# Kernel tuning notes

Measured on AMD Instinct MI355X. Metric: run time of the kernel, lower is better.

## Reference

```python
import jax, jax.numpy as jnp
import numpy as np

B, S, H = 4, 2048, 768
NUM_HEADS = 12
HEAD_DIM = H // NUM_HEADS


def setup_inputs() -> dict:
    key = jax.random.key(0)
    k1, k2, k3 = jax.random.split(key, 3)
    hidden_states = jax.random.normal(k1, (B, S, H), dtype=jnp.float32)
    # torch Linear weight [out,in]; store transposed [in,out] for x @ W
    w_qkv = jax.random.normal(k2, (H, 3 * H), dtype=jnp.float32) * (1.0 / np.sqrt(H))
    w_out = jax.random.normal(k3, (H, H), dtype=jnp.float32) * (1.0 / np.sqrt(H))
    return {"hidden_states": hidden_states, "w_qkv": w_qkv, "w_out": w_out}


def reference(hidden_states, w_qkv, w_out):
    b, s, h = hidden_states.shape
    qkv = hidden_states @ w_qkv                      # [b,s,3h]
    qkv = qkv.reshape(b, s, 3, NUM_HEADS, HEAD_DIM)
    qkv = jnp.transpose(qkv, (2, 0, 3, 1, 4))        # [3,b,nh,s,hd]
    q, k, v = qkv[0], qkv[1], qkv[2]
    scale = 1.0 / np.sqrt(HEAD_DIM).astype(np.float32)
    scores = jnp.einsum('bhqd,bhkd->bhqk', q, k) * scale   # [b,nh,s,s]
    causal = jnp.triu(jnp.ones((s, s), dtype=bool), k=1)
    scores = jnp.where(causal, jnp.float32(-jnp.inf), scores)
    attn = jax.nn.softmax(scores, axis=-1)
    # dropout is identity in eval mode
    out = jnp.einsum('bhqk,bhkd->bhqd', attn, v)      # [b,nh,s,hd]
    out = jnp.transpose(out, (0, 2, 1, 3)).reshape(b, s, h)
    return out @ w_out
```

## Files before the change

### kernel.cpp

```cpp
#include <hip/hip_runtime.h>
#include <stdint.h>

#define B_ 4
#define S_ 2048
#define H_ 768
#define NH_ 12
#define HD_ 64
#define BH_ (B_ * NH_)

#define QSCALE 0.18033688011112042f

typedef __attribute__((ext_vector_type(4))) float f32x4;
typedef __attribute__((ext_vector_type(8))) __bf16 bf16x8;
typedef __attribute__((ext_vector_type(8))) unsigned short ushort8;

__device__ __forceinline__ unsigned short bf16rne(float f) {
  union { float f; unsigned int u; } v;
  v.f = f;
  unsigned int u = v.u;
  return (unsigned short)((u + 0x7fffu + ((u >> 16) & 1u)) >> 16);
}

#if __has_builtin(__builtin_amdgcn_cvt_pk_bf16_f32)
__device__ __forceinline__ unsigned int pk2(float a, float b) {
  auto r = __builtin_amdgcn_cvt_pk_bf16_f32(a, b);
  return *(unsigned int*)&r;
}
#else
__device__ __forceinline__ unsigned int pk2(float a, float b) {
  return (unsigned int)bf16rne(a) | ((unsigned int)bf16rne(b) << 16);
}
#endif

#if __has_builtin(__builtin_amdgcn_exp2f)
#define EXP2F(x) __builtin_amdgcn_exp2f(x)
#else
#define EXP2F(x) exp2f(x)
#endif

__device__ __forceinline__ void gll16(const void* g, void* l) {
  __builtin_amdgcn_global_load_lds(
      (const __attribute__((address_space(1))) unsigned int*)g,
      (__attribute__((address_space(3))) unsigned int*)l, 16, 0, 0);
}

__device__ __forceinline__ void tconv_body(const float* __restrict__ in,
                                           unsigned short* __restrict__ out,
                                           int R, int C, int bx, int by,
                                           unsigned short (*tile)[72], int tid) {
  int c0 = bx * 64, r0 = by * 64;
#pragma unroll
  for (int i = 0; i < 4; ++i) {
    int c = i * 256 + tid;
    int row = c >> 4, col4 = (c & 15) * 4;
    float4 v = *(const float4*)(in + (size_t)(r0 + row) * C + c0 + col4);
    *(uint2*)(&tile[row][col4]) = (uint2){pk2(v.x, v.y), pk2(v.z, v.w)};
  }
  __syncthreads();
#pragma unroll
  for (int i = 0; i < 2; ++i) {
    int c = i * 256 + tid;
    int oc = c >> 3, r8 = (c & 7) * 8;
    ushort8 v;
#pragma unroll
    for (int j = 0; j < 8; ++j) v[j] = tile[r8 + j][oc];
    *(ushort8*)(out + (size_t)(c0 + oc) * R + r0 + r8) = v;
  }
}

__global__ __launch_bounds__(256) void prep_kernel(const float* __restrict__ hs,
                                                   const float* __restrict__ wqkv,
                                                   const float* __restrict__ wout,
                                                   unsigned short* __restrict__ Xbf,
                                                   unsigned short* __restrict__ Wqkvt,
                                                   unsigned short* __restrict__ Woutt) {
  __shared__ unsigned short tile[64][72];
  int bid = blockIdx.x, tid = threadIdx.x;
  if (bid < 3072) {
    int i = (bid * 256 + tid) * 8;
    const float4* p = (const float4*)(hs + i);
    float4 a = p[0], b = p[1];
    uint4 r = {pk2(a.x, a.y), pk2(a.z, a.w), pk2(b.x, b.y), pk2(b.z, b.w)};
    *(uint4*)(Xbf + i) = r;
  } else if (bid < 3504) {
    int idx = bid - 3072;
    tconv_body(wqkv, Wqkvt, 768, 2304, idx % 36, idx / 36, tile, tid);
  } else {
    int idx = bid - 3504;
    tconv_body(wout, Woutt, 768, 768, idx % 12, idx / 12, tile, tid);
  }
}

template <int MODE>
__device__ __forceinline__ void gemm_core(const unsigned short* __restrict__ A,
                                          const unsigned short* __restrict__ Bm,
                                          void* __restrict__ Cout, int N, int K,
                                          int bm, int bn,
                                          unsigned short* As, unsigned short* Bs) {
  int tid = threadIdx.x;
  int lane = tid & 63, wave = tid >> 6;
  int quad = lane >> 4, l16 = lane & 15;
  int wm = (wave & 1) * 64, wn = (wave >> 1) * 64;
  const unsigned short* Ag = A + (size_t)bm * 128 * K;
  const unsigned short* Bg = Bm + (size_t)bn * 128 * K;

  f32x4 zero = {0.f, 0.f, 0.f, 0.f};
  f32x4 acc[4][4];
#pragma unroll
  for (int mt = 0; mt < 4; ++mt)
#pragma unroll
    for (int nt = 0; nt < 4; ++nt) acc[mt][nt] = zero;

  for (int k0 = 0; k0 < K; k0 += 32) {
#pragma unroll
    for (int i = 0; i < 2; ++i) {
      int c = i * 256 + tid;
      int row = c >> 2, off = (c & 3) * 8;
      gll16(Ag + (size_t)row * K + k0 + off, As + c * 8);
      gll16(Bg + (size_t)row * K + k0 + off, Bs + c * 8);
    }
    __syncthreads();
    bf16x8 af[4], bf[4];
#pragma unroll
    for (int mt = 0; mt < 4; ++mt)
      af[mt] = *(const bf16x8*)(As + (wm + mt * 16 + l16) * 32 + quad * 8);
#pragma unroll
    for (int nt = 0; nt < 4; ++nt)
      bf[nt] = *(const bf16x8*)(Bs + (wn + nt * 16 + l16) * 32 + quad * 8);
#pragma unroll
    for (int mt = 0; mt < 4; ++mt)
#pragma unroll
      for (int nt = 0; nt < 4; ++nt) {
        if (MODE == 2)
          acc[mt][nt] = __builtin_amdgcn_mfma_f32_16x16x32_bf16(af[mt], bf[nt], acc[mt][nt], 0, 0, 0);
        else
          acc[mt][nt] = __builtin_amdgcn_mfma_f32_16x16x32_bf16(bf[nt], af[mt], acc[mt][nt], 0, 0, 0);
      }
    __syncthreads();
  }

  if (MODE == 0) {
    unsigned short* qkv = (unsigned short*)Cout;
    int which = (bn >= 6);
#pragma unroll
    for (int mt = 0; mt < 4; ++mt)
#pragma unroll
      for (int nt = 0; nt < 4; ++nt) {
        int f0 = bn * 128 + wn + nt * 16 + quad * 4;
        int tm = bm * 128 + wm + mt * 16 + l16;
        int rem = f0 - which * 768;
        int head = rem >> 6, d0 = rem & 63;
        int b = tm >> 11, s = tm & 2047;
        if (which == 0) {
          uint2 pkv = {pk2(acc[mt][nt][0] * QSCALE, acc[mt][nt][1] * QSCALE),
                       pk2(acc[mt][nt][2] * QSCALE, acc[mt][nt][3] * QSCALE)};
          *(uint2*)(qkv + (((size_t)b * NH_ + head) * S_ + s) * HD_ + d0) = pkv;
        } else {
          uint2 pkv = {pk2(acc[mt][nt][0], acc[mt][nt][1]),
                       pk2(acc[mt][nt][2], acc[mt][nt][3])};
          int dd0 = (((d0 >> 3) ^ (s & 7)) << 3) | (d0 & 7);
          *(uint2*)(qkv + (((size_t)(BH_ + b * NH_ + head)) * S_ + s) * HD_ + dd0) = pkv;
        }
      }
  } else if (MODE == 2) {
    unsigned short* vt = (unsigned short*)Cout;
#pragma unroll
    for (int mt = 0; mt < 4; ++mt)
#pragma unroll
      for (int nt = 0; nt < 4; ++nt) {
        int f = bn * 128 + wn + nt * 16 + l16;
        int t0 = bm * 128 + wm + mt * 16 + quad * 4;
        int rem = f - 1536;
        int head = rem >> 6, d = rem & 63;
        int b = t0 >> 11, s0 = t0 & 2047;
        int tile = s0 >> 6, sin = s0 & 63;
        int pos = (((sin >> 3) ^ (d & 7)) << 3) | (sin & 7);
        uint2 pkv = {pk2(acc[mt][nt][0], acc[mt][nt][1]),
                     pk2(acc[mt][nt][2], acc[mt][nt][3])};
        *(uint2*)(vt + (((size_t)(b * NH_ + head)) * HD_ + d) * S_ + tile * 64 + pos) = pkv;
      }
  } else {
    float* outp = (float*)Cout;
#pragma unroll
    for (int mt = 0; mt < 4; ++mt)
#pragma unroll
      for (int nt = 0; nt < 4; ++nt) {
        int f0 = bn * 128 + wn + nt * 16 + quad * 4;
        int tm = bm * 128 + wm + mt * 16 + l16;
        *(f32x4*)(outp + (size_t)tm * N + f0) = acc[mt][nt];
      }
  }
}

__global__ __launch_bounds__(256) void gemm_qkv(const unsigned short* __restrict__ A,
                                                const unsigned short* __restrict__ Bm,
                                                unsigned short* __restrict__ QK,
                                                unsigned short* __restrict__ Vt) {
  __shared__ unsigned short As[128 * 32];
  __shared__ unsigned short Bs[128 * 32];
  int bm = blockIdx.x, bn = blockIdx.y;
  if (bn < 12)
    gemm_core<0>(A, Bm, QK, 2304, 768, bm, bn, As, Bs);
  else
    gemm_core<2>(A, Bm, Vt, 2304, 768, bm, bn, As, Bs);
}

__global__ __launch_bounds__(256) void gemm_out(const unsigned short* __restrict__ A,
                                                const unsigned short* __restrict__ Bm,
                                                float* __restrict__ Cout) {
  __shared__ unsigned short As[128 * 32];
  __shared__ unsigned short Bs[128 * 32];
  gemm_core<1>(A, Bm, Cout, 768, 768, blockIdx.x, blockIdx.y, As, Bs);
}

__global__ __launch_bounds__(512, 6) void attn_kernel(const unsigned short* __restrict__ Q,
                                                      const unsigned short* __restrict__ Kg,
                                                      const unsigned short* __restrict__ Vt,
                                                      unsigned short* __restrict__ O) {
  __shared__ unsigned short Ks[2][64 * 64];
  __shared__ unsigned short Vs[2][64 * 64];
  __shared__ unsigned short Ps[8][16 * 64];
  const int pi_[16] = {0, 1, 3, 5, 7, 9, 11, 13, 15, 14, 12, 10, 8, 6, 4, 2};
  int bh = blockIdx.x;
  int y = blockIdx.y;
  int qt = pi_[(bh + y) & 15];
  int tid = threadIdx.x, lane = tid & 63, wave = tid >> 6;
  int quad = lane >> 4, l16 = lane & 15;
  const unsigned short* Qp = Q + (size_t)bh * S_ * HD_;
  int q0 = qt * 128;
  int qrow = q0 + wave * 16 + l16;
  int kmax_w = (q0 + wave * 16 + 15) >> 6;
  int kmax_b = 2 * qt + 1;

  const unsigned short* kSrc = Kg + (size_t)bh * S_ * HD_ + (tid >> 3) * HD_ + (tid & 7) * 8;
  const unsigned short* vSrc = Vt + (size_t)bh * HD_ * S_ + (size_t)(tid >> 3) * S_ + (tid & 7) * 8;
  unsigned short* kDst = &Ks[0][tid * 8];
  unsigned short* vDst = &Vs[0][tid * 8];

  auto stage = [&](int t, int buf) {
    gll16(kSrc + (size_t)t * 4096, kDst + buf * 4096);
    gll16(vSrc + t * 64, vDst + buf * 4096);
  };

  stage(0, 0);

  bf16x8 qf[2];
#pragma unroll
  for (int ks = 0; ks < 2; ++ks)
    qf[ks] = *(const bf16x8*)(Qp + (size_t)qrow * HD_ + ks * 32 + quad * 8);

  bf16x8 ones;
#pragma unroll
  for (int j = 0; j < 8; ++j) ones[j] = (__bf16)1.0f;

  int fo[8];
#pragma unroll
  for (int ks = 0; ks < 2; ++ks)
#pragma unroll
    for (int nt = 0; nt < 4; ++nt)
      fo[ks * 4 + nt] = (nt * 16 + l16) * 64 + (((ks * 4 + quad) ^ (l16 & 7)) << 3);
  int po[2];
#pragma unroll
  for (int ks = 0; ks < 2; ++ks)
    po[ks] = l16 * 64 + (((ks * 4 + quad) ^ (l16 & 7)) << 3);
  int pw[4];
#pragma unroll
  for (int nt = 0; nt < 4; ++nt)
    pw[nt] = l16 * 64 + ((((nt * 2 + (quad >> 1)) ^ (l16 & 7)) << 3) | ((quad & 1) * 4));
  unsigned short* psW = &Ps[wave][0];

  f32x4 zero = {0.f, 0.f, 0.f, 0.f};
  float l_i = 0.f;
  f32x4 o[4];
#pragma unroll
  for (int nt = 0; nt < 4; ++nt) o[nt] = zero;

  auto body = [&](int t, const unsigned short* Kb, const unsigned short* Vb) {
    f32x4 sf[4];
#pragma unroll
    for (int nt = 0; nt < 4; ++nt) sf[nt] = zero;
#pragma unroll
    for (int ks = 0; ks < 2; ++ks)
#pragma unroll
      for (int nt = 0; nt < 4; ++nt) {
        bf16x8 kf = *(const bf16x8*)(Kb + fo[ks * 4 + nt]);
        sf[nt] = __builtin_amdgcn_mfma_f32_16x16x32_bf16(kf, qf[ks], sf[nt], 0, 0, 0);
      }

    if (t == kmax_w) {
#pragma unroll
      for (int nt = 0; nt < 4; ++nt)
#pragma unroll
        for (int r = 0; r < 4; ++r)
          if (t * 64 + nt * 16 + quad * 4 + r > qrow) sf[nt][r] = -1e30f;
    }

#pragma unroll
    for (int nt = 0; nt < 4; ++nt) {
      uint2 pkv = {pk2(EXP2F(sf[nt][0]), EXP2F(sf[nt][1])),
                   pk2(EXP2F(sf[nt][2]), EXP2F(sf[nt][3]))};
      *(uint2*)(psW + pw[nt]) = pkv;
    }

    f32x4 rsv = zero;
#pragma unroll
    for (int ks = 0; ks < 2; ++ks) {
      bf16x8 pf = *(const bf16x8*)(psW + po[ks]);
      rsv = __builtin_amdgcn_mfma_f32_16x16x32_bf16(ones, pf, rsv, 0, 0, 0);
#pragma unroll
      for (int nt = 0; nt < 4; ++nt) {
        bf16x8 vf = *(const bf16x8*)(Vb + fo[ks * 4 + nt]);
        o[nt] = __builtin_amdgcn_mfma_f32_16x16x32_bf16(vf, pf, o[nt], 0, 0, 0);
      }
    }
    l_i += rsv[0];
  };

  for (int t = 0; t <= kmax_b; t += 2) {
    __syncthreads();
    stage(t + 1, 1);
    if (t <= kmax_w) body(t, &Ks[0][0], &Vs[0][0]);
    __syncthreads();
    if (t + 2 <= kmax_b) stage(t + 2, 0);
    if (t + 1 <= kmax_w) body(t + 1, &Ks[1][0], &Vs[1][0]);
  }

  float inv = 1.f / l_i;
  int b = bh / NH_, h = bh % NH_;
#pragma unroll
  for (int nt = 0; nt < 4; ++nt) {
    uint2 pkv = {pk2(o[nt][0] * inv, o[nt][1] * inv),
                 pk2(o[nt][2] * inv, o[nt][3] * inv)};
    int d0 = nt * 16 + quad * 4;
    *(uint2*)(O + ((size_t)b * S_ + qrow) * H_ + h * HD_ + d0) = pkv;
  }
}

extern "C" void kernel_launch(void* const* d_in, const int* in_sizes, int n_in,
                              void* d_out, int out_size, void* d_ws, size_t ws_size,
                              hipStream_t stream) {
  (void)in_sizes; (void)n_in; (void)out_size; (void)ws_size;
  const float* hs = (const float*)d_in[0];
  const float* wqkv = (const float*)d_in[1];
  const float* wout = (const float*)d_in[2];
  float* out = (float*)d_out;

  unsigned short* Xbf = (unsigned short*)d_ws;
  unsigned short* Wqkvt = Xbf + (size_t)8192 * 768;
  unsigned short* Woutt = Wqkvt + (size_t)2304 * 768;
  unsigned short* QK = Woutt + (size_t)768 * 768;
  unsigned short* Vt = QK + (size_t)2 * BH_ * S_ * HD_;
  unsigned short* Attn = Xbf;

  prep_kernel<<<3648, 256, 0, stream>>>(hs, wqkv, wout, Xbf, Wqkvt, Woutt);
  gemm_qkv<<<dim3(64, 18), 256, 0, stream>>>(Xbf, Wqkvt, QK, Vt);
  attn_kernel<<<dim3(48, 16), 512, 0, stream>>>(QK, QK + (size_t)BH_ * S_ * HD_, Vt, Attn);
  gemm_out<<<dim3(64, 6), 256, 0, stream>>>(Attn, Woutt, out);
}
```

Before: 197.9 us.

## Split attention key tiles across wave pairs and balance causal work with paired query tiles

The attention kernel now uses 64-row query tiles, and each block processes two of them (y and 31-y), so every block does about the same amount of causal work. Within a tile, pairs of waves split each 64-key block into halves, and the partial outputs and row sums are combined through shared memory at the end. This removes the lookup-table tile permutation and the per-wave uneven kmax handling. In exchange it adds a shared-memory reduction, extra barriers, and a barrier on every key tile. The launch grid must match 16 y-blocks per head, which is not shown.

```diff
diff --git a/kernel.cpp b/kernel.cpp
--- a/kernel.cpp
+++ b/kernel.cpp
@@ -217,38 +217,28 @@
                                                       const unsigned short* __restrict__ Kg,
                                                       const unsigned short* __restrict__ Vt,
                                                       unsigned short* __restrict__ O) {
-  __shared__ unsigned short Ks[2][64 * 64];
-  __shared__ unsigned short Vs[2][64 * 64];
-  __shared__ unsigned short Ps[8][16 * 64];
-  const int pi_[16] = {0, 1, 3, 5, 7, 9, 11, 13, 15, 14, 12, 10, 8, 6, 4, 2};
+  __shared__ __align__(16) unsigned short smem[24576];
+  unsigned short* Ks = smem;
+  unsigned short* Vs = smem + 8192;
+  unsigned short* Ps = smem + 16384;
+
   int bh = blockIdx.x;
   int y = blockIdx.y;
-  int qt = pi_[(bh + y) & 15];
   int tid = threadIdx.x, lane = tid & 63, wave = tid >> 6;
   int quad = lane >> 4, l16 = lane & 15;
+  int grp = wave >> 1, par = wave & 1;
   const unsigned short* Qp = Q + (size_t)bh * S_ * HD_;
-  int q0 = qt * 128;
-  int qrow = q0 + wave * 16 + l16;
-  int kmax_w = (q0 + wave * 16 + 15) >> 6;
-  int kmax_b = 2 * qt + 1;
 
   const unsigned short* kSrc = Kg + (size_t)bh * S_ * HD_ + (tid >> 3) * HD_ + (tid & 7) * 8;
   const unsigned short* vSrc = Vt + (size_t)bh * HD_ * S_ + (size_t)(tid >> 3) * S_ + (tid & 7) * 8;
-  unsigned short* kDst = &Ks[0][tid * 8];
-  unsigned short* vDst = &Vs[0][tid * 8];
+  unsigned short* kDst = &Ks[tid * 8];
+  unsigned short* vDst = &Vs[tid * 8];
 
   auto stage = [&](int t, int buf) {
     gll16(kSrc + (size_t)t * 4096, kDst + buf * 4096);
     gll16(vSrc + t * 64, vDst + buf * 4096);
   };
 
-  stage(0, 0);
-
-  bf16x8 qf[2];
-#pragma unroll
-  for (int ks = 0; ks < 2; ++ks)
-    qf[ks] = *(const bf16x8*)(Qp + (size_t)qrow * HD_ + ks * 32 + quad * 8);
-
   bf16x8 ones;
 #pragma unroll
   for (int j = 0; j < 8; ++j) ones[j] = (__bf16)1.0f;
@@ -259,80 +249,99 @@
 #pragma unroll
     for (int nt = 0; nt < 4; ++nt)
       fo[ks * 4 + nt] = (nt * 16 + l16) * 64 + (((ks * 4 + quad) ^ (l16 & 7)) << 3);
-  int po[2];
-#pragma unroll
-  for (int ks = 0; ks < 2; ++ks)
-    po[ks] = l16 * 64 + (((ks * 4 + quad) ^ (l16 & 7)) << 3);
-  int pw[4];
-#pragma unroll
-  for (int nt = 0; nt < 4; ++nt)
-    pw[nt] = l16 * 64 + ((((nt * 2 + (quad >> 1)) ^ (l16 & 7)) << 3) | ((quad & 1) * 4));
-  unsigned short* psW = &Ps[wave][0];
+  int po = l16 * 64 + (((par * 4 + quad) ^ (l16 & 7)) << 3);
+  int pw[2];
+#pragma unroll
+  for (int ntl = 0; ntl < 2; ++ntl) {
+    int ntp = par * 2 + ntl;
+    pw[ntl] = l16 * 64 + ((((ntp * 2 + (quad >> 1)) ^ (l16 & 7)) << 3) | ((quad & 1) * 4));
+  }
+  unsigned short* psW = &Ps[wave * 1024];
 
   f32x4 zero = {0.f, 0.f, 0.f, 0.f};
-  float l_i = 0.f;
-  f32x4 o[4];
-#pragma unroll
-  for (int nt = 0; nt < 4; ++nt) o[nt] = zero;
-
-  auto body = [&](int t, const unsigned short* Kb, const unsigned short* Vb) {
-    f32x4 sf[4];
-#pragma unroll
-    for (int nt = 0; nt < 4; ++nt) sf[nt] = zero;
+  int b = bh / NH_, h = bh % NH_;
+
+#pragma unroll 1
+  for (int pass = 0; pass < 2; ++pass) {
+    int qt = pass ? (31 - y) : y;
+    int q0 = qt * 64;
+    int qrow = q0 + grp * 16 + l16;
+
+    __syncthreads();
+    stage(0, 0);
+
+    bf16x8 qf[2];
 #pragma unroll
     for (int ks = 0; ks < 2; ++ks)
-#pragma unroll
-      for (int nt = 0; nt < 4; ++nt) {
-        bf16x8 kf = *(const bf16x8*)(Kb + fo[ks * 4 + nt]);
-        sf[nt] = __builtin_amdgcn_mfma_f32_16x16x32_bf16(kf, qf[ks], sf[nt], 0, 0, 0);
-      }
-
-    if (t == kmax_w) {
-#pragma unroll
-      for (int nt = 0; nt < 4; ++nt)
-#pragma unroll
-        for (int r = 0; r < 4; ++r)
-          if (t * 64 + nt * 16 + quad * 4 + r > qrow) sf[nt][r] = -1e30f;
+      qf[ks] = *(const bf16x8*)(Qp + (size_t)qrow * HD_ + ks * 32 + quad * 8);
+
+    f32x4 o[4];
+#pragma unroll
+    for (int nt = 0; nt < 4; ++nt) o[nt] = zero;
+    f32x4 rsum = zero;
+
+    for (int t = 0; t <= qt; ++t) {
+      __syncthreads();
+      if (t < qt) stage(t + 1, (t + 1) & 1);
+      const unsigned short* Kb = Ks + (t & 1) * 4096;
+      const unsigned short* Vb = Vs + (t & 1) * 4096;
+
+      f32x4 sf[2];
+      sf[0] = zero; sf[1] = zero;
+#pragma unroll
+      for (int ks = 0; ks < 2; ++ks)
+#pragma unroll
+        for (int ntl = 0; ntl < 2; ++ntl) {
+          bf16x8 kf = *(const bf16x8*)(Kb + fo[ks * 4 + (par * 2 + ntl)]);
+          sf[ntl] = __builtin_amdgcn_mfma_f32_16x16x32_bf16(kf, qf[ks], sf[ntl], 0, 0, 0);
+        }
+
+      if (t == qt) {
+#pragma unroll
+        for (int ntl = 0; ntl < 2; ++ntl)
+#pragma unroll
+          for (int r = 0; r < 4; ++r)
+            if ((par * 2 + ntl) * 16 + quad * 4 + r > grp * 16 + l16) sf[ntl][r] = -1e30f;
+      }
+
+#pragma unroll
+      for (int ntl = 0; ntl < 2; ++ntl) {
+        uint2 pkv = {pk2(EXP2F(sf[ntl][0]), EXP2F(sf[ntl][1])),
+                     pk2(EXP2F(sf[ntl][2]), EXP2F(sf[ntl][3]))};
+        *(uint2*)(psW + pw[ntl]) = pkv;
+      }
+
+      bf16x8 pf = *(const bf16x8*)(psW + po);
+      rsum = __builtin_amdgcn_mfma_f32_16x16x32_bf16(ones, pf, rsum, 0, 0, 0);
+#pragma unroll
+      for (int nt = 0; nt < 4; ++nt) {
+        bf16x8 vf = *(const bf16x8*)(Vb + fo[par * 4 + nt]);
+        o[nt] = __builtin_amdgcn_mfma_f32_16x16x32_bf16(vf, pf, o[nt], 0, 0, 0);
+      }
     }
-
-#pragma unroll
-    for (int nt = 0; nt < 4; ++nt) {
-      uint2 pkv = {pk2(EXP2F(sf[nt][0]), EXP2F(sf[nt][1])),
-                   pk2(EXP2F(sf[nt][2]), EXP2F(sf[nt][3]))};
-      *(uint2*)(psW + pw[nt]) = pkv;
+    float l = rsum[0];
+
+    __syncthreads();
+    float* sc = (float*)smem + (size_t)(grp * 64 + lane) * 20;
+    if (par) {
+#pragma unroll
+      for (int nt = 0; nt < 4; ++nt) *(f32x4*)(sc + nt * 4) = o[nt];
+      sc[16] = l;
     }
-
-    f32x4 rsv = zero;
-#pragma unroll
-    for (int ks = 0; ks < 2; ++ks) {
-      bf16x8 pf = *(const bf16x8*)(psW + po[ks]);
-      rsv = __builtin_amdgcn_mfma_f32_16x16x32_bf16(ones, pf, rsv, 0, 0, 0);
-#pragma unroll
-      for (int nt = 0; nt < 4; ++nt) {
-        bf16x8 vf = *(const bf16x8*)(Vb + fo[ks * 4 + nt]);
-        o[nt] = __builtin_amdgcn_mfma_f32_16x16x32_bf16(vf, pf, o[nt], 0, 0, 0);
+    __syncthreads();
+    if (!par) {
+#pragma unroll
+      for (int nt = 0; nt < 4; ++nt) o[nt] += *(const f32x4*)(sc + nt * 4);
+      l += sc[16];
+      float inv = 1.f / l;
+#pragma unroll
+      for (int nt = 0; nt < 4; ++nt) {
+        uint2 pkv = {pk2(o[nt][0] * inv, o[nt][1] * inv),
+                     pk2(o[nt][2] * inv, o[nt][3] * inv)};
+        int d0 = nt * 16 + quad * 4;
+        *(uint2*)(O + ((size_t)b * S_ + qrow) * H_ + h * HD_ + d0) = pkv;
       }
     }
-    l_i += rsv[0];
-  };
-
-  for (int t = 0; t <= kmax_b; t += 2) {
-    __syncthreads();
-    stage(t + 1, 1);
-    if (t <= kmax_w) body(t, &Ks[0][0], &Vs[0][0]);
-    __syncthreads();
-    if (t + 2 <= kmax_b) stage(t + 2, 0);
-    if (t + 1 <= kmax_w) body(t + 1, &Ks[1][0], &Vs[1][0]);
-  }
-
-  float inv = 1.f / l_i;
-  int b = bh / NH_, h = bh % NH_;
-#pragma unroll
-  for (int nt = 0; nt < 4; ++nt) {
-    uint2 pkv = {pk2(o[nt][0] * inv, o[nt][1] * inv),
-                 pk2(o[nt][2] * inv, o[nt][3] * inv)};
-    int d0 = nt * 16 + quad * 4;
-    *(uint2*)(O + ((size_t)b * S_ + qrow) * H_ + h * HD_ + d0) = pkv;
   }
 }
 
```

Result: slower. 224.7 us (+13.6%).

## Switch attention to 32x32x16 MFMA with four waves of 32 query rows

Applied to the files above, without the earlier changes.

Rewrites the attention kernel to use 32x32x16 bf16 MFMA tiles instead of 16x16x32. Each of four waves now handles 32 query rows, so a block is 256 threads rather than 512. Staging loads, the P scratch layout, causal masking indices and output writes are remapped to match. The larger tiles raise the MFMA work per LDS fragment load, at the cost of more accumulator registers per thread and fewer waves per block to hide latency.

```diff
diff --git a/kernel.cpp b/kernel.cpp
--- a/kernel.cpp
+++ b/kernel.cpp
@@ -11,6 +11,7 @@
 #define QSCALE 0.18033688011112042f
 
 typedef __attribute__((ext_vector_type(4))) float f32x4;
+typedef __attribute__((ext_vector_type(16))) float f32x16;
 typedef __attribute__((ext_vector_type(8))) __bf16 bf16x8;
 typedef __attribute__((ext_vector_type(8))) unsigned short ushort8;
 
@@ -213,107 +214,105 @@
   gemm_core<1>(A, Bm, Cout, 768, 768, blockIdx.x, blockIdx.y, As, Bs);
 }
 
-__global__ __launch_bounds__(512, 6) void attn_kernel(const unsigned short* __restrict__ Q,
+__global__ __launch_bounds__(256, 3) void attn_kernel(const unsigned short* __restrict__ Q,
                                                       const unsigned short* __restrict__ Kg,
                                                       const unsigned short* __restrict__ Vt,
                                                       unsigned short* __restrict__ O) {
   __shared__ unsigned short Ks[2][64 * 64];
   __shared__ unsigned short Vs[2][64 * 64];
-  __shared__ unsigned short Ps[8][16 * 64];
+  __shared__ unsigned short Ps[4][32 * 64];
   const int pi_[16] = {0, 1, 3, 5, 7, 9, 11, 13, 15, 14, 12, 10, 8, 6, 4, 2};
   int bh = blockIdx.x;
   int y = blockIdx.y;
   int qt = pi_[(bh + y) & 15];
   int tid = threadIdx.x, lane = tid & 63, wave = tid >> 6;
-  int quad = lane >> 4, l16 = lane & 15;
+  int l32 = lane & 31, h = lane >> 5;
   const unsigned short* Qp = Q + (size_t)bh * S_ * HD_;
   int q0 = qt * 128;
-  int qrow = q0 + wave * 16 + l16;
-  int kmax_w = (q0 + wave * 16 + 15) >> 6;
+  int qrow = q0 + wave * 32 + l32;
+  int kmax_w = (q0 + wave * 32 + 31) >> 6;
   int kmax_b = 2 * qt + 1;
 
-  const unsigned short* kSrc = Kg + (size_t)bh * S_ * HD_ + (tid >> 3) * HD_ + (tid & 7) * 8;
-  const unsigned short* vSrc = Vt + (size_t)bh * HD_ * S_ + (size_t)(tid >> 3) * S_ + (tid & 7) * 8;
-  unsigned short* kDst = &Ks[0][tid * 8];
-  unsigned short* vDst = &Vs[0][tid * 8];
+  const unsigned short* kS = Kg + (size_t)bh * S_ * HD_ + (tid >> 3) * HD_ + (tid & 7) * 8;
+  const unsigned short* vS = Vt + (size_t)bh * HD_ * S_ + (size_t)(tid >> 3) * S_ + (tid & 7) * 8;
 
   auto stage = [&](int t, int buf) {
-    gll16(kSrc + (size_t)t * 4096, kDst + buf * 4096);
-    gll16(vSrc + t * 64, vDst + buf * 4096);
+#pragma unroll
+    for (int i = 0; i < 2; ++i) {
+      gll16(kS + i * 32 * HD_ + (size_t)t * 4096, &Ks[buf][(i * 256 + tid) * 8]);
+      gll16(vS + (size_t)i * 32 * S_ + t * 64, &Vs[buf][(i * 256 + tid) * 8]);
+    }
   };
 
   stage(0, 0);
 
-  bf16x8 qf[2];
-#pragma unroll
-  for (int ks = 0; ks < 2; ++ks)
-    qf[ks] = *(const bf16x8*)(Qp + (size_t)qrow * HD_ + ks * 32 + quad * 8);
+  bf16x8 qf[4];
+#pragma unroll
+  for (int dk = 0; dk < 4; ++dk)
+    qf[dk] = *(const bf16x8*)(Qp + (size_t)qrow * HD_ + dk * 16 + h * 8);
 
   bf16x8 ones;
 #pragma unroll
   for (int j = 0; j < 8; ++j) ones[j] = (__bf16)1.0f;
 
-  int fo[8];
-#pragma unroll
-  for (int ks = 0; ks < 2; ++ks)
-#pragma unroll
-    for (int nt = 0; nt < 4; ++nt)
-      fo[ks * 4 + nt] = (nt * 16 + l16) * 64 + (((ks * 4 + quad) ^ (l16 & 7)) << 3);
-  int po[2];
-#pragma unroll
-  for (int ks = 0; ks < 2; ++ks)
-    po[ks] = l16 * 64 + (((ks * 4 + quad) ^ (l16 & 7)) << 3);
-  int pw[4];
-#pragma unroll
-  for (int nt = 0; nt < 4; ++nt)
-    pw[nt] = l16 * 64 + ((((nt * 2 + (quad >> 1)) ^ (l16 & 7)) << 3) | ((quad & 1) * 4));
+  int fo[2][4];
+#pragma unroll
+  for (int x = 0; x < 2; ++x)
+#pragma unroll
+    for (int yy = 0; yy < 4; ++yy)
+      fo[x][yy] = (x * 32 + l32) * 64 + (((yy * 2 + h) ^ (l32 & 7)) << 3);
+  int pwr[2][4];
+#pragma unroll
+  for (int kb = 0; kb < 2; ++kb)
+#pragma unroll
+    for (int g = 0; g < 4; ++g)
+      pwr[kb][g] = l32 * 64 + ((((kb * 4 + g) ^ (l32 & 7))) << 3) + h * 4;
   unsigned short* psW = &Ps[wave][0];
 
-  f32x4 zero = {0.f, 0.f, 0.f, 0.f};
-  float l_i = 0.f;
-  f32x4 o[4];
-#pragma unroll
-  for (int nt = 0; nt < 4; ++nt) o[nt] = zero;
+  f32x16 zero16;
+#pragma unroll
+  for (int j = 0; j < 16; ++j) zero16[j] = 0.f;
+  f32x16 o[2], rsv;
+  o[0] = zero16; o[1] = zero16; rsv = zero16;
 
   auto body = [&](int t, const unsigned short* Kb, const unsigned short* Vb) {
-    f32x4 sf[4];
-#pragma unroll
-    for (int nt = 0; nt < 4; ++nt) sf[nt] = zero;
-#pragma unroll
-    for (int ks = 0; ks < 2; ++ks)
-#pragma unroll
-      for (int nt = 0; nt < 4; ++nt) {
-        bf16x8 kf = *(const bf16x8*)(Kb + fo[ks * 4 + nt]);
-        sf[nt] = __builtin_amdgcn_mfma_f32_16x16x32_bf16(kf, qf[ks], sf[nt], 0, 0, 0);
+    f32x16 sf[2];
+    sf[0] = zero16; sf[1] = zero16;
+#pragma unroll
+    for (int kb = 0; kb < 2; ++kb)
+#pragma unroll
+      for (int dk = 0; dk < 4; ++dk) {
+        bf16x8 kf = *(const bf16x8*)(Kb + fo[kb][dk]);
+        sf[kb] = __builtin_amdgcn_mfma_f32_32x32x16_bf16(kf, qf[dk], sf[kb], 0, 0, 0);
       }
 
     if (t == kmax_w) {
 #pragma unroll
-      for (int nt = 0; nt < 4; ++nt)
-#pragma unroll
-        for (int r = 0; r < 4; ++r)
-          if (t * 64 + nt * 16 + quad * 4 + r > qrow) sf[nt][r] = -1e30f;
-    }
-
-#pragma unroll
-    for (int nt = 0; nt < 4; ++nt) {
-      uint2 pkv = {pk2(EXP2F(sf[nt][0]), EXP2F(sf[nt][1])),
-                   pk2(EXP2F(sf[nt][2]), EXP2F(sf[nt][3]))};
-      *(uint2*)(psW + pw[nt]) = pkv;
-    }
-
-    f32x4 rsv = zero;
-#pragma unroll
-    for (int ks = 0; ks < 2; ++ks) {
-      bf16x8 pf = *(const bf16x8*)(psW + po[ks]);
-      rsv = __builtin_amdgcn_mfma_f32_16x16x32_bf16(ones, pf, rsv, 0, 0, 0);
-#pragma unroll
-      for (int nt = 0; nt < 4; ++nt) {
-        bf16x8 vf = *(const bf16x8*)(Vb + fo[ks * 4 + nt]);
-        o[nt] = __builtin_amdgcn_mfma_f32_16x16x32_bf16(vf, pf, o[nt], 0, 0, 0);
-      }
-    }
-    l_i += rsv[0];
+      for (int kb = 0; kb < 2; ++kb)
+#pragma unroll
+        for (int r = 0; r < 16; ++r)
+          if (t * 64 + kb * 32 + (r & 3) + 8 * (r >> 2) + 4 * h > qrow) sf[kb][r] = -1e30f;
+    }
+
+#pragma unroll
+    for (int kb = 0; kb < 2; ++kb)
+#pragma unroll
+      for (int g = 0; g < 4; ++g) {
+        uint2 pkv = {pk2(EXP2F(sf[kb][g * 4 + 0]), EXP2F(sf[kb][g * 4 + 1])),
+                     pk2(EXP2F(sf[kb][g * 4 + 2]), EXP2F(sf[kb][g * 4 + 3]))};
+        *(uint2*)(psW + pwr[kb][g]) = pkv;
+      }
+
+#pragma unroll
+    for (int ks = 0; ks < 4; ++ks) {
+      bf16x8 pf = *(const bf16x8*)(psW + fo[0][ks]);
+      rsv = __builtin_amdgcn_mfma_f32_32x32x16_bf16(ones, pf, rsv, 0, 0, 0);
+#pragma unroll
+      for (int db = 0; db < 2; ++db) {
+        bf16x8 vf = *(const bf16x8*)(Vb + fo[db][ks]);
+        o[db] = __builtin_amdgcn_mfma_f32_32x32x16_bf16(vf, pf, o[db], 0, 0, 0);
+      }
+    }
   };
 
   for (int t = 0; t <= kmax_b; t += 2) {
@@ -325,15 +324,17 @@
     if (t + 1 <= kmax_w) body(t + 1, &Ks[1][0], &Vs[1][0]);
   }
 
-  float inv = 1.f / l_i;
-  int b = bh / NH_, h = bh % NH_;
-#pragma unroll
-  for (int nt = 0; nt < 4; ++nt) {
-    uint2 pkv = {pk2(o[nt][0] * inv, o[nt][1] * inv),
-                 pk2(o[nt][2] * inv, o[nt][3] * inv)};
-    int d0 = nt * 16 + quad * 4;
-    *(uint2*)(O + ((size_t)b * S_ + qrow) * H_ + h * HD_ + d0) = pkv;
-  }
+  float inv = 1.f / rsv[0];
+  int b = bh / NH_, hh = bh % NH_;
+#pragma unroll
+  for (int db = 0; db < 2; ++db)
+#pragma unroll
+    for (int g = 0; g < 4; ++g) {
+      uint2 pkv = {pk2(o[db][g * 4 + 0] * inv, o[db][g * 4 + 1] * inv),
+                   pk2(o[db][g * 4 + 2] * inv, o[db][g * 4 + 3] * inv)};
+      int d0 = db * 32 + 8 * g + 4 * h;
+      *(uint2*)(O + ((size_t)b * S_ + qrow) * H_ + hh * HD_ + d0) = pkv;
+    }
 }
 
 extern "C" void kernel_launch(void* const* d_in, const int* in_sizes, int n_in,
@@ -354,6 +355,6 @@
 
   prep_kernel<<<3648, 256, 0, stream>>>(hs, wqkv, wout, Xbf, Wqkvt, Woutt);
   gemm_qkv<<<dim3(64, 18), 256, 0, stream>>>(Xbf, Wqkvt, QK, Vt);
-  attn_kernel<<<dim3(48, 16), 512, 0, stream>>>(QK, QK + (size_t)BH_ * S_ * HD_, Vt, Attn);
+  attn_kernel<<<dim3(48, 16), 256, 0, stream>>>(QK, QK + (size_t)BH_ * S_ * HD_, Vt, Attn);
   gemm_out<<<dim3(64, 6), 256, 0, stream>>>(Attn, Woutt, out);
 }
```

After: 202.8 us. 2.5% more time.
